# Kernel tuning notes

Hardware: AMD Instinct MI355X
Metric: run time of the kernel (lower is better)

The kernel has to match this reference:

```python
import jax, jax.numpy as jnp
import numpy as np

NA = 100000   # authors
NP_ = 100000  # papers
D = 128       # hidden dim
H = 4         # heads
DH = 32       # head dim (D = H*DH)
L = 2         # layers
R = 3         # relations: 0=writes(a->p), 1=rev_writes(p->a), 2=cites(p->p)
E = 400000    # edges per relation
OUT = 40


def setup_inputs() -> dict:
    key = jax.random.key(0)
    ks = jax.random.split(key, 16)
    s = 0.05
    return {
        "x_author": jax.random.normal(ks[0], (NA, D), jnp.float32),
        "x_paper": jax.random.normal(ks[1], (NP_, D), jnp.float32),
        "ei_writes": jax.random.randint(ks[2], (2, E), 0, NA, dtype=jnp.int32),
        "ei_rev": jax.random.randint(ks[3], (2, E), 0, NA, dtype=jnp.int32),
        "ei_cites": jax.random.randint(ks[4], (2, E), 0, NP_, dtype=jnp.int32),
        "proj_w": jax.random.normal(ks[5], (2, D, D), jnp.float32) * s,
        "proj_b": jax.random.normal(ks[6], (2, D), jnp.float32) * s,
        "kqv_w": jax.random.normal(ks[7], (L, 3, 2, D, D), jnp.float32) * s,  # [layer, {k,q,v}, type, D, D]
        "kqv_b": jax.random.normal(ks[8], (L, 3, 2, D), jnp.float32) * s,
        "out_w": jax.random.normal(ks[9], (L, 2, D, D), jnp.float32) * s,
        "out_b": jax.random.normal(ks[10], (L, 2, D), jnp.float32) * s,
        "rel_a": jax.random.normal(ks[11], (L, R, H, DH, DH), jnp.float32) * s,
        "rel_m": jax.random.normal(ks[12], (L, R, H, DH, DH), jnp.float32) * s,
        "p_rel": jnp.ones((L, R, H), jnp.float32),
        "skip": jnp.ones((L, 2), jnp.float32),
        "cls_w": jax.random.normal(ks[13], (D, OUT), jnp.float32) * s,
        "cls_b": jnp.zeros((OUT,), jnp.float32),
    }


def _seg_softmax(sc, dst, n):
    # softmax over incoming edges grouped by destination node; sc: [E,H]
    m = jax.ops.segment_max(sc, dst, num_segments=n)
    m = jnp.where(jnp.isfinite(m), m, 0.0)
    e = jnp.exp(sc - m[dst])
    z = jax.ops.segment_sum(e, dst, num_segments=n)
    return e / (z[dst] + 1e-16)


def _hgt_layer(h_a, h_p, ei_w, ei_r, ei_c, kqv_w, kqv_b, out_w, out_b, rel_a, rel_m, p_rel, skip):
    na, npp = h_a.shape[0], h_p.shape[0]

    def kqv(h, t):
        k = (h @ kqv_w[0, t] + kqv_b[0, t]).reshape(-1, H, DH)
        q = (h @ kqv_w[1, t] + kqv_b[1, t]).reshape(-1, H, DH)
        v = (h @ kqv_w[2, t] + kqv_b[2, t]).reshape(-1, H, DH)
        return k, q, v

    k_a, q_a, v_a = kqv(h_a, 0)
    k_p, q_p, v_p = kqv(h_p, 1)
    scale = 1.0 / jnp.sqrt(jnp.float32(DH))

    def edge_msgs(k_src, v_src, q_dst, ei, r):
        ke = jnp.einsum('ehd,hdf->ehf', k_src[ei[0]], rel_a[r])
        ve = jnp.einsum('ehd,hdf->ehf', v_src[ei[0]], rel_m[r])
        sc = (q_dst[ei[1]] * ke).sum(-1) * p_rel[r] * scale  # [E,H]
        return sc, ve

    # destination = paper: writes (r=0) + cites (r=2); softmax jointly per dst node
    sc_w, ve_w = edge_msgs(k_a, v_a, q_p, ei_w, 0)
    sc_c, ve_c = edge_msgs(k_p, v_p, q_p, ei_c, 2)
    sc_p = jnp.concatenate([sc_w, sc_c], 0)
    ve_p = jnp.concatenate([ve_w, ve_c], 0)
    dst_p = jnp.concatenate([ei_w[1], ei_c[1]], 0)
    al_p = _seg_softmax(sc_p, dst_p, npp)
    agg_p = jax.ops.segment_sum(ve_p * al_p[..., None], dst_p, num_segments=npp).reshape(npp, D)

    # destination = author: rev_writes (r=1)
    sc_r, ve_r = edge_msgs(k_p, v_p, q_a, ei_r, 1)
    al_a = _seg_softmax(sc_r, ei_r[1], na)
    agg_a = jax.ops.segment_sum(ve_r * al_a[..., None], ei_r[1], num_segments=na).reshape(na, D)

    def out_mix(agg, h, t):
        o = jax.nn.gelu(agg, approximate=False) @ out_w[t] + out_b[t]
        s = jax.nn.sigmoid(skip[t])
        return s * o + (1.0 - s) * h

    # HGTNet.forward applies ELU after each HGTConv (dropout is identity in eval mode)
    h_a = jax.nn.elu(out_mix(agg_a, h_a, 0))
    h_p = jax.nn.elu(out_mix(agg_p, h_p, 1))
    return h_a, h_p


def reference(x_author, x_paper, ei_writes, ei_rev, ei_cites, proj_w, proj_b,
              kqv_w, kqv_b, out_w, out_b, rel_a, rel_m, p_rel, skip, cls_w, cls_b):
    h_a = x_author @ proj_w[0] + proj_b[0]
    h_p = x_paper @ proj_w[1] + proj_b[1]
    for l in range(L):
        h_a, h_p = _hgt_layer(h_a, h_p, ei_writes, ei_rev, ei_cites,
                              kqv_w[l], kqv_b[l], out_w[l], out_b[l],
                              rel_a[l], rel_m[l], p_rel[l], skip[l])
    return h_p @ cls_w + cls_b
```

## Files before the change

### kernel.cpp

```cpp
#include <hip/hip_runtime.h>
#include <hip/hip_bf16.h>
#include <math.h>

constexpr int NA  = 100000;
constexpr int NPP = 100000;
constexpr int D   = 128;
constexpr int H   = 4;
constexpr int E   = 400000;
constexpr int R   = 3;
constexpr int L   = 2;
constexpr int NSLOT = 23;
constexpr int SLOT_ELEMS = 8 * 4 * 512;
constexpr int GB2c = (NA + 127) / 128;
constexpr int GAc  = NA / 8;

using s8v = __attribute__((ext_vector_type(8))) short;
using f4v = __attribute__((ext_vector_type(4))) float;
typedef unsigned short ushort_t;

static __device__ __forceinline__ unsigned short f2bf(float f) {
  unsigned u = __float_as_uint(f);
  return (unsigned short)((u + 0x7fffu + ((u >> 16) & 1u)) >> 16);
}
static __device__ __forceinline__ float bf2f(unsigned short s) {
  return __uint_as_float(((unsigned)s) << 16);
}
static __device__ __forceinline__ float klo(int i) {
  return __uint_as_float(((unsigned)i) << 16);
}
static __device__ __forceinline__ float vhi(int i) {
  return __uint_as_float(((unsigned)i) & 0xffff0000u);
}
static __device__ __forceinline__ float gelu_f(float x) {
  return 0.5f * x * (1.0f + erff(x * 0.70710678118654752f));
}
static __device__ __forceinline__ float elu_f(float x) {
  return x > 0.0f ? x : expm1f(x);
}

static __device__ __forceinline__ void load_a2(
    const ushort_t* __restrict__ A, int ar0, int ar1, int ks, int g,
    s8v& a0, s8v& a1) {
  const ushort_t* ap0 = A + (size_t)ar0 * 128 + ks * 32 + g * 4;
  ushort4 u0 = *(const ushort4*)ap0;
  ushort4 u1 = *(const ushort4*)(ap0 + 16);
  a0[0]=(short)u0.x; a0[1]=(short)u0.y; a0[2]=(short)u0.z; a0[3]=(short)u0.w;
  a0[4]=(short)u1.x; a0[5]=(short)u1.y; a0[6]=(short)u1.z; a0[7]=(short)u1.w;
  const ushort_t* ap1 = A + (size_t)ar1 * 128 + ks * 32 + g * 4;
  ushort4 v0 = *(const ushort4*)ap1;
  ushort4 v1 = *(const ushort4*)(ap1 + 16);
  a1[0]=(short)v0.x; a1[1]=(short)v0.y; a1[2]=(short)v0.z; a1[3]=(short)v0.w;
  a1[4]=(short)v1.x; a1[5]=(short)v1.y; a1[6]=(short)v1.z; a1[7]=(short)v1.w;
}

template<bool GELU_A, bool MIX>
__device__ __forceinline__ void dev_gemm8(
    const ushort_t* __restrict__ A, const ushort_t* __restrict__ Bhi,
    const float* __restrict__ bias, ushort_t* __restrict__ Cout,
    const float* __restrict__ skip_ptr, int M, int bx, ushort_t* Bs) {
  for (int i = threadIdx.x; i < 2048; i += 256)
    *(s8v*)&Bs[i * 8] = *(const s8v*)(Bhi + (size_t)i * 8);
  __syncthreads();
  const int lane = threadIdx.x & 63;
  const int wave = threadIdx.x >> 6;
  const int row0 = bx * 128 + wave * 32;
  const int g = lane >> 4, li = lane & 15;
  f4v acc0[8], acc1[8];
#pragma unroll
  for (int ct = 0; ct < 8; ++ct) {
    acc0[ct] = f4v{0.f, 0.f, 0.f, 0.f};
    acc1[ct] = f4v{0.f, 0.f, 0.f, 0.f};
  }
  int ar0 = row0 + li;       if (ar0 >= M) ar0 = M - 1;
  int ar1 = row0 + 16 + li;  if (ar1 >= M) ar1 = M - 1;
#pragma unroll
  for (int ks = 0; ks < 4; ++ks) {
    s8v a0, a1;
    load_a2(A, ar0, ar1, ks, g, a0, a1);
    if (GELU_A) {
#pragma unroll
      for (int i = 0; i < 8; ++i) {
        a0[i] = (short)f2bf(gelu_f(bf2f((unsigned short)a0[i])));
        a1[i] = (short)f2bf(gelu_f(bf2f((unsigned short)a1[i])));
      }
    }
#pragma unroll
    for (int ct = 0; ct < 8; ++ct) {
      s8v bhi = *(const s8v*)&Bs[(ct * 4 + ks) * 512 + lane * 8];
      acc0[ct] = __builtin_amdgcn_mfma_f32_16x16x32_bf16(a0, bhi, acc0[ct], 0, 0, 0);
      acc1[ct] = __builtin_amdgcn_mfma_f32_16x16x32_bf16(a1, bhi, acc1[ct], 0, 0, 0);
    }
  }
  float sskip = 0.f;
  if (MIX) sskip = 1.f / (1.f + __expf(-*skip_ptr));
#pragma unroll
  for (int rf = 0; rf < 2; ++rf) {
#pragma unroll
    for (int ct = 0; ct < 8; ++ct) {
      int col = ct * 16 + li;
      float bv = bias[col];
      f4v a = rf ? acc1[ct] : acc0[ct];
#pragma unroll
      for (int r = 0; r < 4; ++r) {
        int grow = row0 + rf * 16 + g * 4 + r;
        if (grow < M) {
          float v = a[r] + bv;
          size_t off = (size_t)grow * 128 + col;
          if constexpr (MIX) {
            float hprev = bf2f(Cout[off]);
            Cout[off] = f2bf(elu_f(sskip * v + (1.f - sskip) * hprev));
          } else {
            Cout[off] = f2bf(v);
          }
        }
      }
    }
  }
}

__device__ __forceinline__ void dev_gemm_kv(
    const ushort_t* __restrict__ A, const ushort_t* __restrict__ Bkv,
    const float* __restrict__ bias, ushort_t* __restrict__ kvout,
    int M, int bx, int ch, ushort_t* Bs) {
  for (int i = threadIdx.x; i < 2048; i += 256) {
    int kvh = i >> 10, j = i & 1023;
    const ushort_t* src = Bkv + (size_t)kvh * SLOT_ELEMS + ch * 8192 + j * 8;
    *(s8v*)&Bs[kvh * 8192 + j * 8] = *(const s8v*)src;
  }
  __syncthreads();
  const int lane = threadIdx.x & 63;
  const int wave = threadIdx.x >> 6;
  const int row0 = bx * 128 + wave * 32;
  const int g = lane >> 4, li = lane & 15;
  f4v acc0[8], acc1[8];
#pragma unroll
  for (int t = 0; t < 8; ++t) {
    acc0[t] = f4v{0.f, 0.f, 0.f, 0.f};
    acc1[t] = f4v{0.f, 0.f, 0.f, 0.f};
  }
  int ar0 = row0 + li;       if (ar0 >= M) ar0 = M - 1;
  int ar1 = row0 + 16 + li;  if (ar1 >= M) ar1 = M - 1;
#pragma unroll
  for (int ks = 0; ks < 4; ++ks) {
    s8v a0, a1;
    load_a2(A, ar0, ar1, ks, g, a0, a1);
#pragma unroll
    for (int t = 0; t < 4; ++t) {
      s8v kh = *(const s8v*)&Bs[(t * 4 + ks) * 512 + lane * 8];
      acc0[t] = __builtin_amdgcn_mfma_f32_16x16x32_bf16(a0, kh, acc0[t], 0, 0, 0);
      acc1[t] = __builtin_amdgcn_mfma_f32_16x16x32_bf16(a1, kh, acc1[t], 0, 0, 0);
      s8v vh = *(const s8v*)&Bs[8192 + (t * 4 + ks) * 512 + lane * 8];
      acc0[4 + t] = __builtin_amdgcn_mfma_f32_16x16x32_bf16(a0, vh, acc0[4 + t], 0, 0, 0);
      acc1[4 + t] = __builtin_amdgcn_mfma_f32_16x16x32_bf16(a1, vh, acc1[4 + t], 0, 0, 0);
    }
  }
#pragma unroll
  for (int rf = 0; rf < 2; ++rf) {
#pragma unroll
    for (int t = 0; t < 4; ++t) {
      int col = ch * 64 + t * 16 + li;
      float bk = bias[col], bv = bias[128 + col];
#pragma unroll
      for (int r = 0; r < 4; ++r) {
        int grow = row0 + rf * 16 + g * 4 + r;
        if (grow < M) {
          float kvl = rf ? acc1[t][r] : acc0[t][r];
          float vvl = rf ? acc1[4 + t][r] : acc0[4 + t][r];
          ushort2 o;
          o.x = f2bf(kvl + bk);
          o.y = f2bf(vvl + bv);
          *(ushort2*)(kvout + (size_t)grow * 256 + 2 * col) = o;
        }
      }
    }
  }
}

__device__ __forceinline__ void dev_proj(
    const float* __restrict__ A, const ushort_t* __restrict__ Bhi,
    const ushort_t* __restrict__ Blo, const float* __restrict__ bias,
    ushort_t* __restrict__ Cout, int M, int bx, ushort_t* Bs) {
  for (int i = threadIdx.x; i < 4096; i += 256) {
    int half = i >> 11, j = i & 2047;
    const ushort_t* src = (half ? Blo : Bhi) + (size_t)j * 8;
    *(s8v*)&Bs[half * 16384 + j * 8] = *(const s8v*)src;
  }
  __syncthreads();
  const int lane = threadIdx.x & 63;
  const int wave = threadIdx.x >> 6;
  const int row0 = bx * 128 + wave * 32;
  const int g = lane >> 4, li = lane & 15;
  f4v acc0[8], acc1[8];
#pragma unroll
  for (int ct = 0; ct < 8; ++ct) {
    acc0[ct] = f4v{0.f, 0.f, 0.f, 0.f};
    acc1[ct] = f4v{0.f, 0.f, 0.f, 0.f};
  }
  int ar0 = row0 + li;       if (ar0 >= M) ar0 = M - 1;
  int ar1 = row0 + 16 + li;  if (ar1 >= M) ar1 = M - 1;
#pragma unroll
  for (int ks = 0; ks < 4; ++ks) {
    s8v ahi[2], alo[2];
#pragma unroll
    for (int rf = 0; rf < 2; ++rf) {
      int ar = rf ? ar1 : ar0;
      const float* ap = A + (size_t)ar * 128 + ks * 32 + g * 4;
      float4 u0 = *(const float4*)ap;
      float4 u1 = *(const float4*)(ap + 16);
      float x[8] = {u0.x, u0.y, u0.z, u0.w, u1.x, u1.y, u1.z, u1.w};
#pragma unroll
      for (int i = 0; i < 8; ++i) {
        unsigned short h = f2bf(x[i]);
        ahi[rf][i] = (short)h;
        alo[rf][i] = (short)f2bf(x[i] - bf2f(h));
      }
    }
#pragma unroll
    for (int ct = 0; ct < 8; ++ct) {
      const ushort_t* bp = &Bs[(ct * 4 + ks) * 512 + lane * 8];
      s8v bhi = *(const s8v*)bp;
      s8v blo = *(const s8v*)(bp + 16384);
      acc0[ct] = __builtin_amdgcn_mfma_f32_16x16x32_bf16(ahi[0], bhi, acc0[ct], 0, 0, 0);
      acc1[ct] = __builtin_amdgcn_mfma_f32_16x16x32_bf16(ahi[1], bhi, acc1[ct], 0, 0, 0);
      acc0[ct] = __builtin_amdgcn_mfma_f32_16x16x32_bf16(alo[0], bhi, acc0[ct], 0, 0, 0);
      acc1[ct] = __builtin_amdgcn_mfma_f32_16x16x32_bf16(alo[1], bhi, acc1[ct], 0, 0, 0);
      acc0[ct] = __builtin_amdgcn_mfma_f32_16x16x32_bf16(ahi[0], blo, acc0[ct], 0, 0, 0);
      acc1[ct] = __builtin_amdgcn_mfma_f32_16x16x32_bf16(ahi[1], blo, acc1[ct], 0, 0, 0);
    }
  }
#pragma unroll
  for (int rf = 0; rf < 2; ++rf) {
#pragma unroll
    for (int ct = 0; ct < 8; ++ct) {
      int col = ct * 16 + li;
      float bv = bias[col];
      f4v a = rf ? acc1[ct] : acc0[ct];
#pragma unroll
      for (int r = 0; r < 4; ++r) {
        int grow = row0 + rf * 16 + g * 4 + r;
        if (grow < M) Cout[(size_t)grow * 128 + col] = f2bf(a[r] + bv);
      }
    }
  }
}

template<bool TWO>
__device__ __forceinline__ void dev_attn(
    const int* __restrict__ rp1, const int* __restrict__ col1,
    const ushort_t* __restrict__ kv1,
    const int* __restrict__ rp2, const int* __restrict__ col2,
    const ushort_t* __restrict__ kv2,
    const ushort_t* __restrict__ q,
    const float* __restrict__ prel1, const float* __restrict__ prel2,
    ushort_t* __restrict__ aggout, int ablk) {
  int lane = threadIdx.x & 63;
  int wave = threadIdx.x >> 6;
  int half = lane >> 5;
  int l32  = lane & 31;
  int dst  = ablk * 8 + wave * 2 + half;
  int head = l32 >> 3;
  const float scale = 0.17677669529663688f;
  float pr1 = prel1[head] * scale;
  float pr2 = TWO ? prel2[head] * scale : pr1;
  ushort4 qv = *(const ushort4*)(q + (size_t)dst * D + l32 * 4);
  float q0 = bf2f(qv.x), q1 = bf2f(qv.y), q2 = bf2f(qv.z), q3 = bf2f(qv.w);
  int e0a = rp1[dst];
  int d1  = rp1[dst + 1] - e0a;
  int e0b = 0, dt = d1;
  if (TWO) { e0b = rp2[dst]; dt = d1 + (rp2[dst + 1] - e0b); }
  float z = 0.f, a0 = 0.f, a1 = 0.f, a2 = 0.f, a3 = 0.f;
  for (int jj = 0; jj < dt; jj += 4) {
    int4 us[4]; bool vs[4]; float prs[4];
#pragma unroll
    for (int s2 = 0; s2 < 4; ++s2) {
      int idx = jj + s2;
      bool v = idx < dt;
      bool f = (!TWO) || (idx < d1);
      int ci = 0;
      if (v) ci = f ? (e0a + idx) : (e0b + idx - d1);
      int src = f ? col1[ci] : col2[ci];
      const ushort_t* kvp = f ? kv1 : kv2;
      us[s2] = *(const int4*)(kvp + (size_t)src * 256 + l32 * 8);
      vs[s2] = v;
      prs[s2] = f ? pr1 : pr2;
    }
#pragma unroll
    for (int s2 = 0; s2 < 4; ++s2) {
      float p = q0 * klo(us[s2].x) + q1 * klo(us[s2].y)
              + q2 * klo(us[s2].z) + q3 * klo(us[s2].w);
      p += __shfl_xor(p, 1);
      p += __shfl_xor(p, 2);
      p += __shfl_xor(p, 4);
      float e = vs[s2] ? __expf(p * prs[s2]) : 0.f;
      z  += e;
      a0 += e * vhi(us[s2].x);
      a1 += e * vhi(us[s2].y);
      a2 += e * vhi(us[s2].z);
      a3 += e * vhi(us[s2].w);
    }
  }
  float inv = 1.f / (z + 1e-16f);
  ushort4 o;
  o.x = f2bf(a0 * inv);
  o.y = f2bf(a1 * inv);
  o.z = f2bf(a2 * inv);
  o.w = f2bf(a3 * inv);
  *(ushort4*)(aggout + (size_t)dst * D + l32 * 4) = o;
}

__device__ __forceinline__ void dev_count(const int* __restrict__ dst,
                                          int* __restrict__ deg, int bidx) {
  for (int e = bidx * 256 + (int)threadIdx.x; e < E; e += 256 * 256)
    atomicAdd(&deg[dst[e]], 1);
}
__device__ __forceinline__ void dev_fill(const int* __restrict__ ei,
                                         const int* __restrict__ rp,
                                         int* __restrict__ cnt,
                                         int* __restrict__ col, int bidx) {
  const int* dst = ei + E;
  for (int e = bidx * 256 + (int)threadIdx.x; e < E; e += 256 * 256) {
    int d = dst[e];
    int pos = atomicAdd(&cnt[d], 1);
    col[rp[d] + pos] = ei[e];
  }
}

__global__ __launch_bounds__(256, 2) void fusedProj(
    const float* __restrict__ x_a, const float* __restrict__ x_p,
    const ushort_t* __restrict__ B0h, const ushort_t* __restrict__ B0l,
    const ushort_t* __restrict__ B1h, const ushort_t* __restrict__ B1l,
    const float* __restrict__ proj_b,
    ushort_t* __restrict__ h_a, ushort_t* __restrict__ h_p,
    const int* __restrict__ ei_w, const int* __restrict__ ei_c,
    const int* __restrict__ ei_r, int* __restrict__ degz) {
  __shared__ ushort_t Bs[32768];
  unsigned b = blockIdx.x;
  if (b % 3 == 2) {
    int ci = b / 3;
    if (ci < 768) {
      int rel = ci >> 8, sub = ci & 255;
      const int* dst = rel == 0 ? ei_w + E : rel == 1 ? ei_c + E : ei_r + E;
      dev_count(dst, degz + rel * NPP, sub);
    }
  } else {
    int gi = b - (b + 1) / 3;
    if (gi < GB2c) dev_proj(x_a, B0h, B0l, proj_b,     h_a, NA,  gi, Bs);
    else           dev_proj(x_p, B1h, B1l, proj_b + D, h_p, NPP, gi - GB2c, Bs);
  }
}

__device__ __forceinline__ void dev_biggemm_slice(
    int slice, int bx,
    const ushort_t* h_a, const ushort_t* h_p,
    const ushort_t* Bqa, const ushort_t* Bqp,
    const ushort_t* BkvR, const ushort_t* BkvW, const ushort_t* BkvC,
    const float* bqa, const float* bqp,
    const float* cbR, const float* cbW, const float* cbC,
    ushort_t* b_q, ushort_t* b_q2,
    ushort_t* kvR, ushort_t* kvW, ushort_t* kvC, ushort_t* Bs) {
  if (slice == 0)      dev_gemm8<false, false>(h_a, Bqa, bqa, b_q,  nullptr, NA,  bx, Bs);
  else if (slice == 1) dev_gemm8<false, false>(h_p, Bqp, bqp, b_q2, nullptr, NPP, bx, Bs);
  else if (slice <= 3) dev_gemm_kv(h_p, BkvR, cbR, kvR, NPP, bx, slice - 2, Bs);
  else if (slice <= 5) dev_gemm_kv(h_a, BkvW, cbW, kvW, NA,  bx, slice - 4, Bs);
  else                 dev_gemm_kv(h_p, BkvC, cbC, kvC, NPP, bx, slice - 6, Bs);
}

__global__ __launch_bounds__(256, 4) void biggemm(
    const ushort_t* __restrict__ h_a, const ushort_t* __restrict__ h_p,
    const ushort_t* __restrict__ Bqa, const ushort_t* __restrict__ Bqp,
    const ushort_t* __restrict__ BkvR, const ushort_t* __restrict__ BkvW,
    const ushort_t* __restrict__ BkvC,
    const float* __restrict__ bqa, const float* __restrict__ bqp,
    const float* __restrict__ cbR, const float* __restrict__ cbW,
    const float* __restrict__ cbC,
    ushort_t* __restrict__ b_q, ushort_t* __restrict__ b_q2,
    ushort_t* __restrict__ kvR, ushort_t* __restrict__ kvW,
    ushort_t* __restrict__ kvC) {
  __shared__ ushort_t Bs[16384];
  dev_biggemm_slice(blockIdx.y, blockIdx.x, h_a, h_p, Bqa, Bqp, BkvR, BkvW, BkvC,
                    bqa, bqp, cbR, cbW, cbC, b_q, b_q2, kvR, kvW, kvC, Bs);
}

__global__ __launch_bounds__(256, 4) void fusedFill(
    const ushort_t* __restrict__ h_a, const ushort_t* __restrict__ h_p,
    const ushort_t* __restrict__ Bqa, const ushort_t* __restrict__ Bqp,
    const ushort_t* __restrict__ BkvR, const ushort_t* __restrict__ BkvW,
    const ushort_t* __restrict__ BkvC,
    const float* __restrict__ bqa, const float* __restrict__ bqp,
    const float* __restrict__ cbR, const float* __restrict__ cbW,
    const float* __restrict__ cbC,
    ushort_t* __restrict__ b_q, ushort_t* __restrict__ b_q2,
    ushort_t* __restrict__ kvR, ushort_t* __restrict__ kvW,
    ushort_t* __restrict__ kvC,
    const int* __restrict__ ei_w, const int* __restrict__ ei_c,
    const int* __restrict__ ei_r,
    const int* __restrict__ rp_w, const int* __restrict__ rp_c,
    const int* __restrict__ rp_r,
    int* __restrict__ cntz, int* __restrict__ colz) {
  __shared__ ushort_t Bs[16384];
  unsigned b = blockIdx.x;
  if (b % 9 == 8) {
    int fi = b / 9;
    if (fi < 768) {
      int rel = fi >> 8, sub = fi & 255;
      const int* ei = rel == 0 ? ei_w : rel == 1 ? ei_c : ei_r;
      const int* rp = rel == 0 ? rp_w : rel == 1 ? rp_c : rp_r;
      dev_fill(ei, rp, cntz + rel * NPP, colz + rel * E, sub);
    }
  } else {
    int gi = b - (b + 1) / 9;
    int slice = gi & 7, bx = gi >> 3;
    if (bx < GB2c)
      dev_biggemm_slice(slice, bx, h_a, h_p, Bqa, Bqp, BkvR, BkvW, BkvC,
                        bqa, bqp, cbR, cbW, cbC, b_q, b_q2, kvR, kvW, kvC, Bs);
  }
}

__global__ __launch_bounds__(256, 8) void bigattn(
    const int* __restrict__ rp_r, const int* __restrict__ col_r,
    const ushort_t* __restrict__ kvR, ushort_t* __restrict__ q_a,
    const int* __restrict__ rp_w, const int* __restrict__ col_w,
    const ushort_t* __restrict__ kvW,
    const int* __restrict__ rp_c, const int* __restrict__ col_c,
    const ushort_t* __restrict__ kvC, ushort_t* __restrict__ q_p,
    const float* __restrict__ prelR, const float* __restrict__ prelW,
    const float* __restrict__ prelC) {
  unsigned x = blockIdx.x;
  if (x & 1)
    dev_attn<false>(rp_r, col_r, kvR, nullptr, nullptr, nullptr,
                    q_a, prelR, prelR, q_a, (int)(x >> 1));
  else
    dev_attn<true>(rp_w, col_w, kvW, rp_c, col_c, kvC,
                   q_p, prelW, prelC, q_p, (int)(x >> 1));
}

__global__ __launch_bounds__(256, 4) void bigmix(
    const ushort_t* __restrict__ agg_a, const ushort_t* __restrict__ Bo0,
    const float* __restrict__ ob0, ushort_t* __restrict__ h_a,
    const float* __restrict__ sk0,
    const ushort_t* __restrict__ agg_p, const ushort_t* __restrict__ Bo1,
    const float* __restrict__ ob1, ushort_t* __restrict__ h_p,
    const float* __restrict__ sk1) {
  __shared__ ushort_t Bs[16384];
  if (blockIdx.y == 0) dev_gemm8<true, true>(agg_a, Bo0, ob0, h_a, sk0, NA,  blockIdx.x, Bs);
  else                 dev_gemm8<true, true>(agg_p, Bo1, ob1, h_p, sk1, NPP, blockIdx.x, Bs);
}

__global__ __launch_bounds__(256, 4) void gemm_cls(
    const ushort_t* __restrict__ A,
    const ushort_t* __restrict__ Bhi, const ushort_t* __restrict__ Blo,
    const float* __restrict__ bias, float* __restrict__ Cv, int M) {
  constexpr int NT16 = 3;
  constexpr int HN = NT16 * 2048;
  __shared__ ushort_t Bs[HN * 2];
  for (int i = threadIdx.x; i < (HN / 8) * 2; i += 256) {
    int half = i / (HN / 8), j = i % (HN / 8);
    const ushort_t* src = (half ? Blo : Bhi) + (size_t)j * 8;
    *(s8v*)&Bs[half * HN + j * 8] = *(const s8v*)src;
  }
  __syncthreads();
  const int lane = threadIdx.x & 63;
  const int wave = threadIdx.x >> 6;
  const int row0 = blockIdx.x * 128 + wave * 32;
  const int g = lane >> 4, li = lane & 15;
  f4v acc0[NT16], acc1[NT16];
#pragma unroll
  for (int ct = 0; ct < NT16; ++ct) {
    acc0[ct] = f4v{0.f, 0.f, 0.f, 0.f};
    acc1[ct] = f4v{0.f, 0.f, 0.f, 0.f};
  }
  int ar0 = row0 + li;       if (ar0 >= M) ar0 = M - 1;
  int ar1 = row0 + 16 + li;  if (ar1 >= M) ar1 = M - 1;
#pragma unroll
  for (int ks = 0; ks < 4; ++ks) {
    s8v a0, a1;
    load_a2(A, ar0, ar1, ks, g, a0, a1);
#pragma unroll
    for (int ct = 0; ct < NT16; ++ct) {
      const ushort_t* bp = &Bs[(ct * 4 + ks) * 512 + lane * 8];
      s8v bhi = *(const s8v*)bp;
      s8v blo = *(const s8v*)(bp + HN);
      acc0[ct] = __builtin_amdgcn_mfma_f32_16x16x32_bf16(a0, bhi, acc0[ct], 0, 0, 0);
      acc1[ct] = __builtin_amdgcn_mfma_f32_16x16x32_bf16(a1, bhi, acc1[ct], 0, 0, 0);
      acc0[ct] = __builtin_amdgcn_mfma_f32_16x16x32_bf16(a0, blo, acc0[ct], 0, 0, 0);
      acc1[ct] = __builtin_amdgcn_mfma_f32_16x16x32_bf16(a1, blo, acc1[ct], 0, 0, 0);
    }
  }
#pragma unroll
  for (int rf = 0; rf < 2; ++rf) {
#pragma unroll
    for (int ct = 0; ct < NT16; ++ct) {
      int col = ct * 16 + li;
      bool colok = (col < 40);
      float bv = colok ? bias[col] : 0.f;
      f4v a = rf ? acc1[ct] : acc0[ct];
#pragma unroll
      for (int r = 0; r < 4; ++r) {
        int grow = row0 + rf * 16 + g * 4 + r;
        if (grow < M && colok) Cv[(size_t)grow * 40 + col] = a[r] + bv;
      }
    }
  }
}

__global__ __launch_bounds__(256) void combine_w(
    const float* __restrict__ kqv_w, const float* __restrict__ kqv_b,
    const float* __restrict__ rel_a, const float* __restrict__ rel_m,
    float* __restrict__ cw, float* __restrict__ cb) {
  int b  = blockIdx.x;
  int kv = b & 1;
  int r  = (b >> 1) % R;
  int l  = b / (2 * R);
  int t_src = (r == 0) ? 0 : 1;
  int i_w   = (kv == 0) ? 0 : 2;
  const float* W    = kqv_w + ((size_t)((l*3 + i_w)*2 + t_src)) * D * D;
  const float* bvec = kqv_b + ((size_t)((l*3 + i_w)*2 + t_src)) * D;
  const float* rel  = ((kv == 0) ? rel_a : rel_m) + ((size_t)(l*R + r)) * H * 32 * 32;
  float* Cout = cw + (size_t)b * D * D;
  float* cbo  = cb + (size_t)b * D;
  for (int idx = threadIdx.x; idx < D * D; idx += 256) {
    int i = idx / D, j = idx % D;
    int h = j >> 5, f = j & 31;
    const float* relh = rel + h * 32 * 32;
    float sum = 0.f;
#pragma unroll
    for (int d = 0; d < 32; ++d) sum += W[i*D + (h*32 + d)] * relh[d*32 + f];
    Cout[idx] = sum;
  }
  if (threadIdx.x < D) {
    int j = threadIdx.x;
    int h = j >> 5, f = j & 31;
    const float* relh = rel + h * 32 * 32;
    float sum = 0.f;
#pragma unroll
    for (int d = 0; d < 32; ++d) sum += bvec[h*32 + d] * relh[d*32 + f];
    cbo[j] = sum;
  }
}

__global__ __launch_bounds__(256) void pack_b(
    const float* __restrict__ proj_w, const float* __restrict__ kqv_w,
    const float* __restrict__ out_w, const float* __restrict__ cls_w,
    const float* __restrict__ cw,
    ushort_t* __restrict__ phi, ushort_t* __restrict__ plo) {
  int slot = blockIdx.x;
  const float* src; int ncol = 128;
  if (slot == 0) src = proj_w;
  else if (slot == 1) src = proj_w + D * D;
  else if (slot == 22) { src = cls_w; ncol = 40; }
  else {
    int l = (slot - 2) / 10, k = (slot - 2) % 10;
    if (k == 0)      src = kqv_w + ((size_t)((l*3 + 1)*2 + 0)) * D * D;
    else if (k == 1) src = kqv_w + ((size_t)((l*3 + 1)*2 + 1)) * D * D;
    else if (k < 8)  { int idx = k - 2; src = cw + ((size_t)((l*R)*2 + idx)) * D * D; }
    else             src = out_w + ((size_t)(l*2 + (k - 8))) * D * D;
  }
  int nt = (ncol + 15) / 16;
  int total = nt * 4 * 512;
  ushort_t* ph = phi + (size_t)slot * SLOT_ELEMS;
  ushort_t* pl = plo + (size_t)slot * SLOT_ELEMS;
  for (int idx = threadIdx.x; idx < total; idx += 256) {
    int j = idx & 7, lane = (idx >> 3) & 63, ks = (idx >> 9) & 3, ct = idx >> 11;
    int k = 4 * (lane >> 4) + (j & 3) + 16 * (j >> 2) + 32 * ks;
    int n = ct * 16 + (lane & 15);
    float v = (n < ncol) ? src[(size_t)k * ncol + n] : 0.f;
    unsigned short h = f2bf(v);
    ph[idx] = h;
    pl[idx] = f2bf(v - bf2f(h));
  }
}

__global__ __launch_bounds__(256) void scan_partial(const int* __restrict__ degz,
                                                    int* __restrict__ bsum) {
  int blk = blockIdx.x, rel = blk / 25, t25 = blk % 25;
  const int* deg = degz + rel * NPP + t25 * 4096;
  int nrem = min(4096, NPP - t25 * 4096);
  int base = threadIdx.x * 16;
  int s = 0;
  if (base < nrem) {
#pragma unroll
    for (int i4 = 0; i4 < 4; ++i4) {
      int4 v = *(const int4*)(deg + base + i4 * 4);
      s += v.x + v.y + v.z + v.w;
    }
  }
  __shared__ int sm[256];
  sm[threadIdx.x] = s; __syncthreads();
  for (int o = 128; o > 0; o >>= 1) {
    if (threadIdx.x < o) sm[threadIdx.x] += sm[threadIdx.x + o];
    __syncthreads();
  }
  if (threadIdx.x == 0) bsum[blk] = sm[0];
}
__global__ __launch_bounds__(256) void scan_final(const int* __restrict__ degz,
                                                  const int* __restrict__ bsum,
                                                  int* rp_w, int* rp_c, int* rp_r) {
  int blk = blockIdx.x, rel = blk / 25, t25 = blk % 25;
  const int* deg = degz + rel * NPP + t25 * 4096;
  int* rpb = (rel == 0 ? rp_w : rel == 1 ? rp_c : rp_r);
  int* rp = rpb + t25 * 4096;
  int boffv = 0;
  for (int i = 0; i < t25; ++i) boffv += bsum[rel * 25 + i];
  int nrem = min(4096, NPP - t25 * 4096);
  int base = threadIdx.x * 16;
  bool ok = base < nrem;
  int v[16]; int s = 0;
  if (ok) {
#pragma unroll
    for (int i4 = 0; i4 < 4; ++i4) {
      int4 u = *(const int4*)(deg + base + i4 * 4);
      v[i4*4+0] = u.x; v[i4*4+1] = u.y; v[i4*4+2] = u.z; v[i4*4+3] = u.w;
      s += u.x + u.y + u.z + u.w;
    }
  }
  __shared__ int sm[256];
  sm[threadIdx.x] = s; __syncthreads();
  for (int o = 1; o < 256; o <<= 1) {
    int x = (threadIdx.x >= o) ? sm[threadIdx.x - o] : 0;
    __syncthreads(); sm[threadIdx.x] += x; __syncthreads();
  }
  int run = boffv + sm[threadIdx.x] - s;
  if (ok) {
    int w[16];
#pragma unroll
    for (int i = 0; i < 16; ++i) { w[i] = run; run += v[i]; }
#pragma unroll
    for (int i4 = 0; i4 < 4; ++i4) *(int4*)(rp + base + i4 * 4) = *(const int4*)&w[i4*4];
  }
  if (t25 == 24 && threadIdx.x == 255) rpb[NPP] = boffv + sm[255];
}

extern "C" void kernel_launch(void* const* d_in, const int* in_sizes, int n_in,
                              void* d_out, int out_size, void* d_ws, size_t ws_size,
                              hipStream_t stream) {
  const float* x_a    = (const float*)d_in[0];
  const float* x_p    = (const float*)d_in[1];
  const int*   ei_w   = (const int*)d_in[2];
  const int*   ei_r   = (const int*)d_in[3];
  const int*   ei_c   = (const int*)d_in[4];
  const float* proj_w = (const float*)d_in[5];
  const float* proj_b = (const float*)d_in[6];
  const float* kqv_w  = (const float*)d_in[7];
  const float* kqv_b  = (const float*)d_in[8];
  const float* out_w  = (const float*)d_in[9];
  const float* out_b  = (const float*)d_in[10];
  const float* rel_a  = (const float*)d_in[11];
  const float* rel_m  = (const float*)d_in[12];
  const float* p_rel  = (const float*)d_in[13];
  const float* skip   = (const float*)d_in[14];
  const float* cls_w  = (const float*)d_in[15];
  const float* cls_b  = (const float*)d_in[16];
  float* out = (float*)d_out;

  const size_t NF = (size_t)NA * D;
  char* p = (char*)d_ws;
  float* cw = (float*)p;              p += (size_t)12 * D * D * 4;
  float* cb = (float*)p;              p += (size_t)12 * D * 4;
  ushort_t* h_a   = (ushort_t*)p;     p += NF * 2;
  ushort_t* h_p   = (ushort_t*)p;     p += NF * 2;
  ushort_t* b_q   = (ushort_t*)p;     p += NF * 2;
  ushort_t* b_q2  = (ushort_t*)p;     p += NF * 2;
  ushort_t* b_kvR = (ushort_t*)p;     p += 2 * NF * 2;
  ushort_t* b_kvW = (ushort_t*)p;     p += 2 * NF * 2;
  ushort_t* b_kvC = (ushort_t*)p;     p += 2 * NF * 2;
  ushort_t* phi = (ushort_t*)p;       p += (size_t)NSLOT * SLOT_ELEMS * 2;
  ushort_t* plo = (ushort_t*)p;       p += (size_t)NSLOT * SLOT_ELEMS * 2;
  int* rp_w = (int*)p;                p += (NPP + 1) * 4;
  int* rp_c = (int*)p;                p += (NPP + 1) * 4;
  int* rp_r = (int*)p;                p += (NA + 1) * 4;
  int* degz = (int*)p;                p += (size_t)3 * NPP * 4;
  int* cntz = (int*)p;                p += (size_t)3 * NPP * 4;
  int* colz = (int*)p;                p += (size_t)3 * E * 4;
  int* bsum = (int*)p;                p += 128 * 4;
  if (ws_size < (size_t)(p - (char*)d_ws)) return;

  hipMemsetAsync(degz, 0, sizeof(int) * 6 * (size_t)NPP, stream);

  combine_w<<<12, 256, 0, stream>>>(kqv_w, kqv_b, rel_a, rel_m, cw, cb);
  pack_b<<<NSLOT, 256, 0, stream>>>(proj_w, kqv_w, out_w, cls_w, cw, phi, plo);

  auto PH = [&](int s){ return phi + (size_t)s * SLOT_ELEMS; };
  auto PL = [&](int s){ return plo + (size_t)s * SLOT_ELEMS; };

  fusedProj<<<2346, 256, 0, stream>>>(
      x_a, x_p, PH(0), PL(0), PH(1), PL(1), proj_b, h_a, h_p,
      ei_w, ei_c, ei_r, degz);
  scan_partial<<<75, 256, 0, stream>>>(degz, bsum);
  scan_final<<<75, 256, 0, stream>>>(degz, bsum, rp_w, rp_c, rp_r);
  int* col_w = colz;
  int* col_c = colz + E;
  int* col_r = colz + 2 * E;

  for (int l = 0; l < L; ++l) {
    const int SQA = 2 + l * 10 + 0, SQP = 2 + l * 10 + 1;
    auto SKV = [&](int r){ return 2 + l * 10 + 2 + r * 2; };
    const int SO0 = 2 + l * 10 + 8, SO1 = 2 + l * 10 + 9;
    const float* bq_a = kqv_b + ((size_t)((l*3 + 1)*2 + 0)) * D;
    const float* bq_p = kqv_b + ((size_t)((l*3 + 1)*2 + 1)) * D;
    auto CB2 = [&](int r){ return cb + ((size_t)((l*R + r)*2)) * D; };
    const float* prelW = p_rel + (size_t)(l*R + 0) * H;
    const float* prelR = p_rel + (size_t)(l*R + 1) * H;
    const float* prelC = p_rel + (size_t)(l*R + 2) * H;

    if (l == 0) {
      fusedFill<<<7038, 256, 0, stream>>>(
          h_a, h_p, PH(SQA), PH(SQP), PH(SKV(1)), PH(SKV(0)), PH(SKV(2)),
          bq_a, bq_p, CB2(1), CB2(0), CB2(2),
          b_q, b_q2, b_kvR, b_kvW, b_kvC,
          ei_w, ei_c, ei_r, rp_w, rp_c, rp_r, cntz, colz);
    } else {
      biggemm<<<dim3(GB2c, 8), 256, 0, stream>>>(
          h_a, h_p, PH(SQA), PH(SQP), PH(SKV(1)), PH(SKV(0)), PH(SKV(2)),
          bq_a, bq_p, CB2(1), CB2(0), CB2(2),
          b_q, b_q2, b_kvR, b_kvW, b_kvC);
    }
    bigattn<<<2 * GAc, 256, 0, stream>>>(
        rp_r, col_r, b_kvR, b_q,
        rp_w, col_w, b_kvW, rp_c, col_c, b_kvC, b_q2,
        prelR, prelW, prelC);
    bigmix<<<dim3(GB2c, 2), 256, 0, stream>>>(
        b_q,  PH(SO0), out_b + (size_t)(l*2 + 0) * D, h_a, skip + l*2 + 0,
        b_q2, PH(SO1), out_b + (size_t)(l*2 + 1) * D, h_p, skip + l*2 + 1);
  }

  gemm_cls<<<dim3(GB2c, 1), 256, 0, stream>>>(
      h_p, PH(22), PL(22), cls_b, out, NPP);
}
```

Before: 799.9 us.

## Merge writes and cites CSR into one paper-destination graph; drop a split-bf16 MFMA term

Builds one CSR for paper destinations that holds both writes and cites edges. Cites source indices are offset by NA into a single concatenated KV buffer, and the relation scale is chosen per edge from the row index. This removes the two-segment branch logic in the attention loop and one scan pass. Separately, the projection GEMM drops the A-low bf16 term, so it issues fewer MFMAs and conversions at some loss of precision.

```diff
diff --git a/kernel.cpp b/kernel.cpp
--- a/kernel.cpp
+++ b/kernel.cpp
@@ -200,7 +200,7 @@
   int ar1 = row0 + 16 + li;  if (ar1 >= M) ar1 = M - 1;
 #pragma unroll
   for (int ks = 0; ks < 4; ++ks) {
-    s8v ahi[2], alo[2];
+    s8v ahi[2];
 #pragma unroll
     for (int rf = 0; rf < 2; ++rf) {
       int ar = rf ? ar1 : ar0;
@@ -209,11 +209,7 @@
       float4 u1 = *(const float4*)(ap + 16);
       float x[8] = {u0.x, u0.y, u0.z, u0.w, u1.x, u1.y, u1.z, u1.w};
 #pragma unroll
-      for (int i = 0; i < 8; ++i) {
-        unsigned short h = f2bf(x[i]);
-        ahi[rf][i] = (short)h;
-        alo[rf][i] = (short)f2bf(x[i] - bf2f(h));
-      }
+      for (int i = 0; i < 8; ++i) ahi[rf][i] = (short)f2bf(x[i]);
     }
 #pragma unroll
     for (int ct = 0; ct < 8; ++ct) {
@@ -222,8 +218,6 @@
       s8v blo = *(const s8v*)(bp + 16384);
       acc0[ct] = __builtin_amdgcn_mfma_f32_16x16x32_bf16(ahi[0], bhi, acc0[ct], 0, 0, 0);
       acc1[ct] = __builtin_amdgcn_mfma_f32_16x16x32_bf16(ahi[1], bhi, acc1[ct], 0, 0, 0);
-      acc0[ct] = __builtin_amdgcn_mfma_f32_16x16x32_bf16(alo[0], bhi, acc0[ct], 0, 0, 0);
-      acc1[ct] = __builtin_amdgcn_mfma_f32_16x16x32_bf16(alo[1], bhi, acc1[ct], 0, 0, 0);
       acc0[ct] = __builtin_amdgcn_mfma_f32_16x16x32_bf16(ahi[0], blo, acc0[ct], 0, 0, 0);
       acc1[ct] = __builtin_amdgcn_mfma_f32_16x16x32_bf16(ahi[1], blo, acc1[ct], 0, 0, 0);
     }
@@ -244,30 +238,20 @@
   }
 }
 
-template<bool TWO>
-__device__ __forceinline__ void dev_attn(
-    const int* __restrict__ rp1, const int* __restrict__ col1,
-    const ushort_t* __restrict__ kv1,
-    const int* __restrict__ rp2, const int* __restrict__ col2,
-    const ushort_t* __restrict__ kv2,
-    const ushort_t* __restrict__ q,
-    const float* __restrict__ prel1, const float* __restrict__ prel2,
-    ushort_t* __restrict__ aggout, int ablk) {
+template<bool SEL>
+__device__ __forceinline__ void dev_attn_m(
+    const int* __restrict__ rp, const int* __restrict__ col,
+    const ushort_t* __restrict__ kv, const ushort_t* __restrict__ q,
+    float prW, float prC, ushort_t* __restrict__ aggout, int ablk) {
   int lane = threadIdx.x & 63;
   int wave = threadIdx.x >> 6;
   int half = lane >> 5;
   int l32  = lane & 31;
   int dst  = ablk * 8 + wave * 2 + half;
-  int head = l32 >> 3;
-  const float scale = 0.17677669529663688f;
-  float pr1 = prel1[head] * scale;
-  float pr2 = TWO ? prel2[head] * scale : pr1;
   ushort4 qv = *(const ushort4*)(q + (size_t)dst * D + l32 * 4);
   float q0 = bf2f(qv.x), q1 = bf2f(qv.y), q2 = bf2f(qv.z), q3 = bf2f(qv.w);
-  int e0a = rp1[dst];
-  int d1  = rp1[dst + 1] - e0a;
-  int e0b = 0, dt = d1;
-  if (TWO) { e0b = rp2[dst]; dt = d1 + (rp2[dst + 1] - e0b); }
+  int e0 = rp[dst];
+  int dt = rp[dst + 1] - e0;
   float z = 0.f, a0 = 0.f, a1 = 0.f, a2 = 0.f, a3 = 0.f;
   for (int jj = 0; jj < dt; jj += 4) {
     int4 us[4]; bool vs[4]; float prs[4];
@@ -275,14 +259,11 @@
     for (int s2 = 0; s2 < 4; ++s2) {
       int idx = jj + s2;
       bool v = idx < dt;
-      bool f = (!TWO) || (idx < d1);
-      int ci = 0;
-      if (v) ci = f ? (e0a + idx) : (e0b + idx - d1);
-      int src = f ? col1[ci] : col2[ci];
-      const ushort_t* kvp = f ? kv1 : kv2;
-      us[s2] = *(const int4*)(kvp + (size_t)src * 256 + l32 * 8);
+      int ci = e0 + (v ? idx : 0);
+      int row = col[ci];
+      us[s2] = *(const int4*)(kv + (size_t)row * 256 + l32 * 8);
       vs[s2] = v;
-      prs[s2] = f ? pr1 : pr2;
+      prs[s2] = SEL ? ((row >= NA) ? prC : prW) : prW;
     }
 #pragma unroll
     for (int s2 = 0; s2 < 4; ++s2) {
@@ -316,12 +297,12 @@
 __device__ __forceinline__ void dev_fill(const int* __restrict__ ei,
                                          const int* __restrict__ rp,
                                          int* __restrict__ cnt,
-                                         int* __restrict__ col, int bidx) {
+                                         int* __restrict__ col, int bidx, int off) {
   const int* dst = ei + E;
   for (int e = bidx * 256 + (int)threadIdx.x; e < E; e += 256 * 256) {
     int d = dst[e];
     int pos = atomicAdd(&cnt[d], 1);
-    col[rp[d] + pos] = ei[e];
+    col[rp[d] + pos] = ei[e] + off;
   }
 }
 
@@ -340,7 +321,8 @@
     if (ci < 768) {
       int rel = ci >> 8, sub = ci & 255;
       const int* dst = rel == 0 ? ei_w + E : rel == 1 ? ei_c + E : ei_r + E;
-      dev_count(dst, degz + rel * NPP, sub);
+      int* deg = (rel == 2) ? (degz + NPP) : degz;
+      dev_count(dst, deg, sub);
     }
   } else {
     int gi = b - (b + 1) / 3;
@@ -357,12 +339,12 @@
     const float* bqa, const float* bqp,
     const float* cbR, const float* cbW, const float* cbC,
     ushort_t* b_q, ushort_t* b_q2,
-    ushort_t* kvR, ushort_t* kvW, ushort_t* kvC, ushort_t* Bs) {
+    ushort_t* kvR, ushort_t* kvP, ushort_t* Bs) {
   if (slice == 0)      dev_gemm8<false, false>(h_a, Bqa, bqa, b_q,  nullptr, NA,  bx, Bs);
   else if (slice == 1) dev_gemm8<false, false>(h_p, Bqp, bqp, b_q2, nullptr, NPP, bx, Bs);
   else if (slice <= 3) dev_gemm_kv(h_p, BkvR, cbR, kvR, NPP, bx, slice - 2, Bs);
-  else if (slice <= 5) dev_gemm_kv(h_a, BkvW, cbW, kvW, NA,  bx, slice - 4, Bs);
-  else                 dev_gemm_kv(h_p, BkvC, cbC, kvC, NPP, bx, slice - 6, Bs);
+  else if (slice <= 5) dev_gemm_kv(h_a, BkvW, cbW, kvP, NA,  bx, slice - 4, Bs);
+  else                 dev_gemm_kv(h_p, BkvC, cbC, kvP + (size_t)NA * 256, NPP, bx, slice - 6, Bs);
 }
 
 __global__ __launch_bounds__(256, 4) void biggemm(
@@ -374,11 +356,10 @@
     const float* __restrict__ cbR, const float* __restrict__ cbW,
     const float* __restrict__ cbC,
     ushort_t* __restrict__ b_q, ushort_t* __restrict__ b_q2,
-    ushort_t* __restrict__ kvR, ushort_t* __restrict__ kvW,
-    ushort_t* __restrict__ kvC) {
+    ushort_t* __restrict__ kvR, ushort_t* __restrict__ kvP) {
   __shared__ ushort_t Bs[16384];
   dev_biggemm_slice(blockIdx.y, blockIdx.x, h_a, h_p, Bqa, Bqp, BkvR, BkvW, BkvC,
-                    bqa, bqp, cbR, cbW, cbC, b_q, b_q2, kvR, kvW, kvC, Bs);
+                    bqa, bqp, cbR, cbW, cbC, b_q, b_q2, kvR, kvP, Bs);
 }
 
 __global__ __launch_bounds__(256, 4) void fusedFill(
@@ -390,48 +371,47 @@
     const float* __restrict__ cbR, const float* __restrict__ cbW,
     const float* __restrict__ cbC,
     ushort_t* __restrict__ b_q, ushort_t* __restrict__ b_q2,
-    ushort_t* __restrict__ kvR, ushort_t* __restrict__ kvW,
-    ushort_t* __restrict__ kvC,
+    ushort_t* __restrict__ kvR, ushort_t* __restrict__ kvP,
     const int* __restrict__ ei_w, const int* __restrict__ ei_c,
     const int* __restrict__ ei_r,
-    const int* __restrict__ rp_w, const int* __restrict__ rp_c,
-    const int* __restrict__ rp_r,
-    int* __restrict__ cntz, int* __restrict__ colz) {
+    const int* __restrict__ rp_p, const int* __restrict__ rp_r,
+    int* __restrict__ cntz, int* __restrict__ col_p, int* __restrict__ col_r) {
   __shared__ ushort_t Bs[16384];
   unsigned b = blockIdx.x;
   if (b % 9 == 8) {
     int fi = b / 9;
     if (fi < 768) {
       int rel = fi >> 8, sub = fi & 255;
-      const int* ei = rel == 0 ? ei_w : rel == 1 ? ei_c : ei_r;
-      const int* rp = rel == 0 ? rp_w : rel == 1 ? rp_c : rp_r;
-      dev_fill(ei, rp, cntz + rel * NPP, colz + rel * E, sub);
+      if (rel == 0)      dev_fill(ei_w, rp_p, cntz,       col_p, sub, 0);
+      else if (rel == 1) dev_fill(ei_c, rp_p, cntz,       col_p, sub, NA);
+      else               dev_fill(ei_r, rp_r, cntz + NPP, col_r, sub, 0);
     }
   } else {
     int gi = b - (b + 1) / 9;
     int slice = gi & 7, bx = gi >> 3;
     if (bx < GB2c)
       dev_biggemm_slice(slice, bx, h_a, h_p, Bqa, Bqp, BkvR, BkvW, BkvC,
-                        bqa, bqp, cbR, cbW, cbC, b_q, b_q2, kvR, kvW, kvC, Bs);
+                        bqa, bqp, cbR, cbW, cbC, b_q, b_q2, kvR, kvP, Bs);
   }
 }
 
 __global__ __launch_bounds__(256, 8) void bigattn(
     const int* __restrict__ rp_r, const int* __restrict__ col_r,
     const ushort_t* __restrict__ kvR, ushort_t* __restrict__ q_a,
-    const int* __restrict__ rp_w, const int* __restrict__ col_w,
-    const ushort_t* __restrict__ kvW,
-    const int* __restrict__ rp_c, const int* __restrict__ col_c,
-    const ushort_t* __restrict__ kvC, ushort_t* __restrict__ q_p,
+    const int* __restrict__ rp_p, const int* __restrict__ col_p,
+    const ushort_t* __restrict__ kvP, ushort_t* __restrict__ q_p,
     const float* __restrict__ prelR, const float* __restrict__ prelW,
     const float* __restrict__ prelC) {
   unsigned x = blockIdx.x;
-  if (x & 1)
-    dev_attn<false>(rp_r, col_r, kvR, nullptr, nullptr, nullptr,
-                    q_a, prelR, prelR, q_a, (int)(x >> 1));
-  else
-    dev_attn<true>(rp_w, col_w, kvW, rp_c, col_c, kvC,
-                   q_p, prelW, prelC, q_p, (int)(x >> 1));
+  int head = (threadIdx.x & 31) >> 3;
+  const float scale = 0.17677669529663688f;
+  if (x & 1) {
+    float pr = prelR[head] * scale;
+    dev_attn_m<false>(rp_r, col_r, kvR, q_a, pr, pr, q_a, (int)(x >> 1));
+  } else {
+    dev_attn_m<true>(rp_p, col_p, kvP, q_p,
+                     prelW[head] * scale, prelC[head] * scale, q_p, (int)(x >> 1));
+  }
 }
 
 __global__ __launch_bounds__(256, 4) void bigmix(
@@ -594,10 +574,10 @@
 }
 __global__ __launch_bounds__(256) void scan_final(const int* __restrict__ degz,
                                                   const int* __restrict__ bsum,
-                                                  int* rp_w, int* rp_c, int* rp_r) {
+                                                  int* rp_p, int* rp_r) {
   int blk = blockIdx.x, rel = blk / 25, t25 = blk % 25;
   const int* deg = degz + rel * NPP + t25 * 4096;
-  int* rpb = (rel == 0 ? rp_w : rel == 1 ? rp_c : rp_r);
+  int* rpb = (rel == 0 ? rp_p : rp_r);
   int* rp = rpb + t25 * 4096;
   int boffv = 0;
   for (int i = 0; i < t25; ++i) boffv += bsum[rel * 25 + i];
@@ -661,20 +641,19 @@
   ushort_t* b_q   = (ushort_t*)p;     p += NF * 2;
   ushort_t* b_q2  = (ushort_t*)p;     p += NF * 2;
   ushort_t* b_kvR = (ushort_t*)p;     p += 2 * NF * 2;
-  ushort_t* b_kvW = (ushort_t*)p;     p += 2 * NF * 2;
-  ushort_t* b_kvC = (ushort_t*)p;     p += 2 * NF * 2;
+  ushort_t* b_kvP = (ushort_t*)p;     p += 4 * NF * 2;
   ushort_t* phi = (ushort_t*)p;       p += (size_t)NSLOT * SLOT_ELEMS * 2;
   ushort_t* plo = (ushort_t*)p;       p += (size_t)NSLOT * SLOT_ELEMS * 2;
-  int* rp_w = (int*)p;                p += (NPP + 1) * 4;
-  int* rp_c = (int*)p;                p += (NPP + 1) * 4;
+  int* rp_p = (int*)p;                p += (NPP + 1) * 4;
   int* rp_r = (int*)p;                p += (NA + 1) * 4;
-  int* degz = (int*)p;                p += (size_t)3 * NPP * 4;
-  int* cntz = (int*)p;                p += (size_t)3 * NPP * 4;
-  int* colz = (int*)p;                p += (size_t)3 * E * 4;
+  int* degz = (int*)p;                p += (size_t)2 * NPP * 4;
+  int* cntz = (int*)p;                p += (size_t)2 * NPP * 4;
+  int* col_p = (int*)p;               p += (size_t)2 * E * 4;
+  int* col_r = (int*)p;               p += (size_t)E * 4;
   int* bsum = (int*)p;                p += 128 * 4;
   if (ws_size < (size_t)(p - (char*)d_ws)) return;
 
-  hipMemsetAsync(degz, 0, sizeof(int) * 6 * (size_t)NPP, stream);
+  hipMemsetAsync(degz, 0, sizeof(int) * 4 * (size_t)NPP, stream);
 
   combine_w<<<12, 256, 0, stream>>>(kqv_w, kqv_b, rel_a, rel_m, cw, cb);
   pack_b<<<NSLOT, 256, 0, stream>>>(proj_w, kqv_w, out_w, cls_w, cw, phi, plo);
@@ -685,11 +664,8 @@
   fusedProj<<<2346, 256, 0, stream>>>(
       x_a, x_p, PH(0), PL(0), PH(1), PL(1), proj_b, h_a, h_p,
       ei_w, ei_c, ei_r, degz);
-  scan_partial<<<75, 256, 0, stream>>>(degz, bsum);
-  scan_final<<<75, 256, 0, stream>>>(degz, bsum, rp_w, rp_c, rp_r);
-  int* col_w = colz;
-  int* col_c = colz + E;
-  int* col_r = colz + 2 * E;
+  scan_partial<<<50, 256, 0, stream>>>(degz, bsum);
+  scan_final<<<50, 256, 0, stream>>>(degz, bsum, rp_p, rp_r);
 
   for (int l = 0; l < L; ++l) {
     const int SQA = 2 + l * 10 + 0, SQP = 2 + l * 10 + 1;
@@ -706,17 +682,17 @@
       fusedFill<<<7038, 256, 0, stream>>>(
           h_a, h_p, PH(SQA), PH(SQP), PH(SKV(1)), PH(SKV(0)), PH(SKV(2)),
           bq_a, bq_p, CB2(1), CB2(0), CB2(2),
-          b_q, b_q2, b_kvR, b_kvW, b_kvC,
-          ei_w, ei_c, ei_r, rp_w, rp_c, rp_r, cntz, colz);
+          b_q, b_q2, b_kvR, b_kvP,
+          ei_w, ei_c, ei_r, rp_p, rp_r, cntz, col_p, col_r);
     } else {
       biggemm<<<dim3(GB2c, 8), 256, 0, stream>>>(
           h_a, h_p, PH(SQA), PH(SQP), PH(SKV(1)), PH(SKV(0)), PH(SKV(2)),
           bq_a, bq_p, CB2(1), CB2(0), CB2(2),
-          b_q, b_q2, b_kvR, b_kvW, b_kvC);
+          b_q, b_q2, b_kvR, b_kvP);
     }
     bigattn<<<2 * GAc, 256, 0, stream>>>(
         rp_r, col_r, b_kvR, b_q,
-        rp_w, col_w, b_kvW, rp_c, col_c, b_kvC, b_q2,
+        rp_p, col_p, b_kvP, b_q2,
         prelR, prelW, prelC);
     bigmix<<<dim3(GB2c, 2), 256, 0, stream>>>(
         b_q,  PH(SO0), out_b + (size_t)(l*2 + 0) * D, h_a, skip + l*2 + 0,
```

Measured after the change: 781.9 us. 2.3% less time.
